# Optimization experiments

Measured on AMD Instinct MI355X. Metric: run time of the kernel, lower is better.

The kernel has to match this reference:

```python
import jax, jax.numpy as jnp
import numpy as np

D_MODEL = 2048
NUM_EXPERTS = 64
TOP_K = 2
N_TOKENS = 16384


def setup_inputs() -> dict:
    key = jax.random.key(0)
    kx, kw = jax.random.split(key)
    x = jax.random.normal(kx, (N_TOKENS, D_MODEL), dtype=jnp.float32)
    # match nn.Linear default init scale roughly (not bit-exact; math is what matters)
    W = jax.random.normal(kw, (D_MODEL, NUM_EXPERTS), dtype=jnp.float32) * (1.0 / np.sqrt(D_MODEL))
    b = jnp.zeros((NUM_EXPERTS,), dtype=jnp.float32)
    return {"x": x, "W": W, "b": b}


def reference(x, W, b):
    # eval-mode forward (self.training False => no noise)
    logits = jnp.einsum("td,de->te", x, W) + b          # [T, E]
    weights = jax.nn.softmax(logits, axis=-1)             # [T, E]
    topk_weights, topk_indices = jax.lax.top_k(weights, TOP_K)  # [T, k] each
    return topk_weights, topk_indices, weights
```

## Files before the change

kernel.cpp:

```cpp
#include <hip/hip_runtime.h>
#include <math.h>


#define T_TOK 16384
#define DMOD  2048
#define NEXP  64
#define NKS   64

typedef __attribute__((ext_vector_type(8))) short short8;
typedef __attribute__((ext_vector_type(4))) float f32x4;

#define MFMA16 __builtin_amdgcn_mfma_f32_16x16x32_bf16

__device__ __forceinline__ unsigned short bf16_rne(float f) {
  unsigned int u = __float_as_uint(f);
  unsigned int r = (u + 0x7fffu + ((u >> 16) & 1u)) >> 16;
  return (unsigned short)r;
}
__device__ __forceinline__ float bf16_up(unsigned short h) {
  return __uint_as_float(((unsigned int)h) << 16);
}

__device__ __forceinline__ void split3_pair(float v0, float v1, unsigned& hp,
                                            unsigned& mp, unsigned& lp) {
  const unsigned short h0 = bf16_rne(v0), h1 = bf16_rne(v1);
  const float e0 = v0 - bf16_up(h0), e1 = v1 - bf16_up(h1);
  const unsigned short m0 = bf16_rne(e0), m1 = bf16_rne(e1);
  const float g0 = e0 - bf16_up(m0), g1 = e1 - bf16_up(m1);
  const unsigned short l0 = bf16_rne(g0), l1 = bf16_rne(g1);
  hp = (unsigned)h0 | ((unsigned)h1 << 16);
  mp = (unsigned)m0 | ((unsigned)m1 << 16);
  lp = (unsigned)l0 | ((unsigned)l1 << 16);
}

__global__ __launch_bounds__(256) void wconv_kernel(
    const float* __restrict__ W, unsigned short* __restrict__ wp) {
  const int tid = blockIdx.x * 256 + threadIdx.x;
  const int l = tid & 63;
  const int g = tid >> 6;
  const int q = l >> 4, c = l & 15;
  const int ks = g >> 2, nt = g & 3;
  const int k0 = ks * 32 + q * 8;
  const int n = nt * 16 + c;
  float v[8];
#pragma unroll
  for (int j = 0; j < 8; ++j) v[j] = W[(size_t)(k0 + j) * NEXP + n];
  uint4 h, m, lo;
  split3_pair(v[0], v[1], h.x, m.x, lo.x);
  split3_pair(v[2], v[3], h.y, m.y, lo.y);
  split3_pair(v[4], v[5], h.z, m.z, lo.z);
  split3_pair(v[6], v[7], h.w, m.w, lo.w);
  unsigned short* base = wp + (size_t)g * 1536 + l * 8;
  *(uint4*)(base) = h;
  *(uint4*)(base + 512) = m;
  *(uint4*)(base + 1024) = lo;
}

__global__ __launch_bounds__(64) void gating_kernel(
    const float* __restrict__ x, const unsigned short* __restrict__ wp,
    const float* __restrict__ bias, float* __restrict__ out) {
  __shared__ float lg[16 * 65];
  __shared__ float red_m[16];
  __shared__ float red_s[16];

  const int l = threadIdx.x;
  const int q = l >> 4, c = l & 15;
  const int t0 = blockIdx.x * 16;

  const float* xg = x + (size_t)(t0 + c) * DMOD + q * 8;
  const unsigned short* wl = wp + l * 8;

  float bv[4];
#pragma unroll
  for (int nt = 0; nt < 4; ++nt) bv[nt] = bias[nt * 16 + c];

  f32x4 acc[4];
#pragma unroll
  for (int nt = 0; nt < 4; ++nt) acc[nt] = (f32x4){0.f, 0.f, 0.f, 0.f};

  float4 xr[4][2];
  short8 bb[2][12];

#pragma unroll
  for (int i = 0; i < 4; ++i) {
    xr[i][0] = *(const float4*)(xg + i * 32);
    xr[i][1] = *(const float4*)(xg + i * 32 + 4);
  }
#pragma unroll
  for (int i = 0; i < 12; ++i) {
    bb[0][i] = *(const short8*)(wl + (size_t)i * 512);
    bb[1][i] = *(const short8*)(wl + (size_t)(12 + i) * 512);
  }

  for (int blk = 0; blk < 16; ++blk) {
#pragma unroll
    for (int u = 0; u < 4; ++u) {
      const int ks = blk * 4 + u;
      short8 ah, am, al;
      {
        uint4 h, m, lo;
        split3_pair(xr[u][0].x, xr[u][0].y, h.x, m.x, lo.x);
        split3_pair(xr[u][0].z, xr[u][0].w, h.y, m.y, lo.y);
        split3_pair(xr[u][1].x, xr[u][1].y, h.z, m.z, lo.z);
        split3_pair(xr[u][1].z, xr[u][1].w, h.w, m.w, lo.w);
        ah = *(short8*)&h;
        am = *(short8*)&m;
        al = *(short8*)&lo;
      }
      {
        const int kn = (ks + 4 < NKS) ? ks + 4 : NKS - 1;
        xr[u][0] = *(const float4*)(xg + kn * 32);
        xr[u][1] = *(const float4*)(xg + kn * 32 + 4);
      }
      const int pb = u & 1;
#pragma unroll
      for (int nt = 0; nt < 4; ++nt) {
        const short8 bh = bb[pb][nt * 3 + 0];
        const short8 bm = bb[pb][nt * 3 + 1];
        const short8 bl = bb[pb][nt * 3 + 2];
        acc[nt] = MFMA16(ah, bh, acc[nt], 0, 0, 0);
        acc[nt] = MFMA16(ah, bm, acc[nt], 0, 0, 0);
        acc[nt] = MFMA16(am, bh, acc[nt], 0, 0, 0);
        acc[nt] = MFMA16(am, bm, acc[nt], 0, 0, 0);
        acc[nt] = MFMA16(ah, bl, acc[nt], 0, 0, 0);
        acc[nt] = MFMA16(al, bh, acc[nt], 0, 0, 0);
      }
      {
        const int kn = (ks + 2 < NKS) ? ks + 2 : NKS - 1;
        const unsigned short* src = wl + (size_t)kn * 6144;
#pragma unroll
        for (int i = 0; i < 12; ++i)
          bb[pb][i] = *(const short8*)(src + (size_t)i * 512);
      }
    }
  }

#pragma unroll
  for (int nt = 0; nt < 4; ++nt)
#pragma unroll
    for (int r = 0; r < 4; ++r)
      lg[(q * 4 + r) * 65 + nt * 16 + c] = acc[nt][r] + bv[nt];
  __syncthreads();

  {
    const int row = l >> 2;
    const int s = l & 3;
    const float* lr = lg + row * 65 + s * 16;
    float mx = -INFINITY;
#pragma unroll
    for (int e = 0; e < 16; ++e) mx = fmaxf(mx, lr[e]);
    mx = fmaxf(mx, __shfl_xor(mx, 1));
    mx = fmaxf(mx, __shfl_xor(mx, 2));
    float sum = 0.f, b1 = -INFINITY, b2 = -INFINITY;
    int i1 = 0, i2 = 0;
#pragma unroll
    for (int e = 0; e < 16; ++e) {
      const float v = lr[e];
      sum += expf(v - mx);
      const int idx = s * 16 + e;
      if (v > b1) {
        b2 = b1; i2 = i1; b1 = v; i1 = idx;
      } else if (v > b2) {
        b2 = v; i2 = idx;
      }
    }
#pragma unroll
    for (int msk = 1; msk <= 2; msk <<= 1) {
      sum += __shfl_xor(sum, msk);
      const float ob1 = __shfl_xor(b1, msk);
      const int oi1 = __shfl_xor(i1, msk);
      const float ob2 = __shfl_xor(b2, msk);
      const int oi2 = __shfl_xor(i2, msk);
      float n1, n2;
      int j1, j2;
      const bool aFirst = (b1 > ob1) || (b1 == ob1 && i1 < oi1);
      if (aFirst) {
        n1 = b1; j1 = i1;
        const bool t = (b2 > ob1) || (b2 == ob1 && i2 < oi1);
        n2 = t ? b2 : ob1; j2 = t ? i2 : oi1;
      } else {
        n1 = ob1; j1 = oi1;
        const bool t = (ob2 > b1) || (ob2 == b1 && oi2 < i1);
        n2 = t ? ob2 : b1; j2 = t ? oi2 : i1;
      }
      b1 = n1; i1 = j1; b2 = n2; i2 = j2;
    }
    if (s == 0) {
      const float inv = 1.f / sum;
      const int t = t0 + row;
      float2 wv, iv;
      wv.x = expf(b1 - mx) * inv;
      wv.y = expf(b2 - mx) * inv;
      iv.x = (float)i1;
      iv.y = (float)i2;
      *(float2*)(out + 2 * t) = wv;
      *(float2*)(out + 2 * T_TOK + 2 * t) = iv;
      red_m[row] = mx;
      red_s[row] = inv;
    }
  }
  __syncthreads();

#pragma unroll
  for (int it = 0; it < 16; ++it) {
    out[4 * T_TOK + (size_t)(t0 + it) * NEXP + l] =
        expf(lg[it * 65 + l] - red_m[it]) * red_s[it];
  }
}

extern "C" void kernel_launch(void* const* d_in, const int* in_sizes, int n_in,
                              void* d_out, int out_size, void* d_ws,
                              size_t ws_size, hipStream_t stream) {
  const float* x = (const float*)d_in[0];
  const float* W = (const float*)d_in[1];
  const float* b = (const float*)d_in[2];
  float* out = (float*)d_out;
  unsigned short* wp = (unsigned short*)d_ws;
  wconv_kernel<<<dim3(64), dim3(256), 0, stream>>>(W, wp);
  gating_kernel<<<dim3(T_TOK / 16), dim3(64), 0, stream>>>(x, wp, b, out);
}
```

Baseline: 232.6 us.

## Split K dimension across four waves per block with LDS reduction

Each 16-token block now uses 256 threads. The four waves each handle one quarter of the 2048-wide reduction dimension, and their partial logits are summed through shared memory before the softmax and top-k step. The goal is to cut the long serial K loop per wave and raise the number of waves in flight, which should hide memory latency on x and the split weights. The cost is extra LDS traffic, one more barrier, and idle waves during the single-wave top-k phase.

```diff
diff --git a/kernel.cpp b/kernel.cpp
--- a/kernel.cpp
+++ b/kernel.cpp
@@ -5,7 +5,7 @@
 #define T_TOK 16384
 #define DMOD  2048
 #define NEXP  64
-#define NKS   64
+#define NKSW  16
 
 typedef __attribute__((ext_vector_type(8))) short short8;
 typedef __attribute__((ext_vector_type(4))) float f32x4;
@@ -56,23 +56,22 @@
   *(uint4*)(base + 1024) = lo;
 }
 
-__global__ __launch_bounds__(64) void gating_kernel(
+__global__ __launch_bounds__(256, 4) void gating_kernel(
     const float* __restrict__ x, const unsigned short* __restrict__ wp,
     const float* __restrict__ bias, float* __restrict__ out) {
-  __shared__ float lg[16 * 65];
+  __shared__ float partial[4 * 16 * 65];
   __shared__ float red_m[16];
   __shared__ float red_s[16];
-
-  const int l = threadIdx.x;
+  float* lg = partial;
+
+  const int tid = threadIdx.x;
+  const int l = tid & 63;
+  const int w = tid >> 6;
   const int q = l >> 4, c = l & 15;
   const int t0 = blockIdx.x * 16;
 
-  const float* xg = x + (size_t)(t0 + c) * DMOD + q * 8;
-  const unsigned short* wl = wp + l * 8;
-
-  float bv[4];
-#pragma unroll
-  for (int nt = 0; nt < 4; ++nt) bv[nt] = bias[nt * 16 + c];
+  const float* xg = x + (size_t)(t0 + c) * DMOD + w * 512 + q * 8;
+  const unsigned short* wl = wp + (size_t)(w * NKSW) * 6144 + l * 8;
 
   f32x4 acc[4];
 #pragma unroll
@@ -92,7 +91,7 @@
     bb[1][i] = *(const short8*)(wl + (size_t)(12 + i) * 512);
   }
 
-  for (int blk = 0; blk < 16; ++blk) {
+  for (int blk = 0; blk < 4; ++blk) {
 #pragma unroll
     for (int u = 0; u < 4; ++u) {
       const int ks = blk * 4 + u;
@@ -108,7 +107,7 @@
         al = *(short8*)&lo;
       }
       {
-        const int kn = (ks + 4 < NKS) ? ks + 4 : NKS - 1;
+        const int kn = (ks + 4 < NKSW) ? ks + 4 : NKSW - 1;
         xr[u][0] = *(const float4*)(xg + kn * 32);
         xr[u][1] = *(const float4*)(xg + kn * 32 + 4);
       }
@@ -126,7 +125,7 @@
         acc[nt] = MFMA16(al, bh, acc[nt], 0, 0, 0);
       }
       {
-        const int kn = (ks + 2 < NKS) ? ks + 2 : NKS - 1;
+        const int kn = (ks + 2 < NKSW) ? ks + 2 : NKSW - 1;
         const unsigned short* src = wl + (size_t)kn * 6144;
 #pragma unroll
         for (int i = 0; i < 12; ++i)
@@ -139,10 +138,22 @@
   for (int nt = 0; nt < 4; ++nt)
 #pragma unroll
     for (int r = 0; r < 4; ++r)
-      lg[(q * 4 + r) * 65 + nt * 16 + c] = acc[nt][r] + bv[nt];
+      partial[w * 1040 + (q * 4 + r) * 65 + nt * 16 + c] = acc[nt][r];
   __syncthreads();
 
-  {
+#pragma unroll
+  for (int r2 = 0; r2 < 4; ++r2) {
+    const int idx = r2 * 256 + tid;
+    const int tt = idx >> 6;
+    const int e = idx & 63;
+    const int o = tt * 65 + e;
+    const float s =
+        partial[o] + partial[1040 + o] + partial[2080 + o] + partial[3120 + o];
+    lg[o] = s + bias[e];
+  }
+  __syncthreads();
+
+  if (tid < 64) {
     const int row = l >> 2;
     const int s = l & 3;
     const float* lr = lg + row * 65 + s * 16;
@@ -202,9 +213,12 @@
   __syncthreads();
 
 #pragma unroll
-  for (int it = 0; it < 16; ++it) {
-    out[4 * T_TOK + (size_t)(t0 + it) * NEXP + l] =
-        expf(lg[it * 65 + l] - red_m[it]) * red_s[it];
+  for (int r2 = 0; r2 < 4; ++r2) {
+    const int idx = r2 * 256 + tid;
+    const int tt = idx >> 6;
+    const int e = idx & 63;
+    out[4 * T_TOK + (size_t)(t0 + tt) * NEXP + e] =
+        expf(lg[tt * 65 + e] - red_m[tt]) * red_s[tt];
   }
 }
 
@@ -217,5 +231,5 @@
   float* out = (float*)d_out;
   unsigned short* wp = (unsigned short*)d_ws;
   wconv_kernel<<<dim3(64), dim3(256), 0, stream>>>(W, wp);
-  gating_kernel<<<dim3(T_TOK / 16), dim3(64), 0, stream>>>(x, wp, b, out);
-}
+  gating_kernel<<<dim3(T_TOK / 16), dim3(256), 0, stream>>>(x, wp, b, out);
+}
```

New measurement: 371.0 us. 1.6x slower.
